# Performance work log

Measured on AMD Instinct MI355X. Metric: run time of the kernel, lower is better.

The kernel has to match this reference:

```python
import jax, jax.numpy as jnp
import numpy as np

N_NODES = 50000
N_EDGES = 500000
D_IN = 128
D_HID = 128
OUTPUT_DIM = 10.0


def gcn_conv(x, src, dst, edge_weight, W, b, n_nodes):
    # PyG GCNConv: out = D^{-1/2} (A + I) D^{-1/2} X W + b, self-loop weight 1
    xw = x @ W  # [N, D_out]
    # degree at target nodes, including self-loop weight 1
    deg = jax.ops.segment_sum(edge_weight, dst, num_segments=n_nodes) + 1.0
    dinv = jnp.where(deg > 0, jax.lax.rsqrt(deg), 0.0)  # [N]
    norm = dinv[src] * edge_weight * dinv[dst]  # [E]
    msgs = xw[src] * norm[:, None]  # [E, D_out] gathered+scaled messages
    agg = jax.ops.segment_sum(msgs, dst, num_segments=n_nodes)
    # analytic self-loop contribution: norm_ii = dinv_i * 1 * dinv_i
    agg = agg + xw * (dinv * dinv)[:, None]
    return agg + b


def setup_inputs() -> dict:
    key = jax.random.key(0)
    k = jax.random.split(key, 8)
    x = jax.random.normal(k[0], (N_NODES, D_IN), dtype=jnp.float32)
    edge_index = jax.random.randint(k[1], (2, N_EDGES), 0, N_NODES, dtype=jnp.int64)
    edge_weight = jax.random.uniform(k[2], (N_EDGES,), dtype=jnp.float32)
    s1 = 1.0 / np.sqrt(D_IN)
    s2 = 1.0 / np.sqrt(D_HID)
    W1 = jax.random.uniform(k[3], (D_IN, D_HID), minval=-s1, maxval=s1, dtype=jnp.float32)
    b1 = jnp.zeros((D_HID,), dtype=jnp.float32)
    W2 = jax.random.uniform(k[4], (D_HID, D_HID), minval=-s2, maxval=s2, dtype=jnp.float32)
    b2 = jnp.zeros((D_HID,), dtype=jnp.float32)
    Wf = jax.random.uniform(k[5], (D_HID, 1), minval=-s2, maxval=s2, dtype=jnp.float32)
    bf = jax.random.uniform(k[6], (1,), minval=-s2, maxval=s2, dtype=jnp.float32)
    return {"x": x, "edge_index": edge_index, "edge_weight": edge_weight,
            "W1": W1, "b1": b1, "W2": W2, "b2": b2, "Wf": Wf, "bf": bf}


def reference(x, edge_index, edge_weight, W1, b1, W2, b2, Wf, bf):
    src, dst = edge_index[0], edge_index[1]
    h = gcn_conv(x, src, dst, edge_weight, W1, b1, N_NODES)
    h = gcn_conv(h, src, dst, edge_weight, W2, b2, N_NODES)
    out = h @ Wf + bf  # [N, 1]
    return jax.nn.sigmoid(out) * OUTPUT_DIM
```

## Files before the change

### kernel.cpp

```cpp
#include <hip/hip_runtime.h>

#define N_NODES 50000
#define N_EDGES 500000
#define D 128
#define FXS 4194304.0f
#define CAP 64

typedef unsigned long long u64;

__global__ void pass1_kernel(const int* __restrict__ src, const int* __restrict__ dst,
                             const float* __restrict__ ew,
                             const float* __restrict__ W1, const float* __restrict__ W2,
                             const float* __restrict__ b1, const float* __restrict__ b2,
                             const float* __restrict__ Wf, const float* __restrict__ bf,
                             u64* __restrict__ degcnt, int2* __restrict__ pairs,
                             float* __restrict__ v, float* __restrict__ consts,
                             int eb) {
    if ((int)blockIdx.x == eb) {
        __shared__ float u[D];
        int t = threadIdx.x;
        if (t < D) {
            float a = 0.f;
#pragma unroll 8
            for (int j = 0; j < D; ++j) a += W2[t * D + j] * Wf[j];
            u[t] = a;
        }
        __syncthreads();
        if (t < D) {
            float a = 0.f;
#pragma unroll 8
            for (int k = 0; k < D; ++k) a += W1[t * D + k] * u[k];
            v[t] = a;
        }
        if (t == 0) {
            float c = 0.f;
            for (int k = 0; k < D; ++k) c += b1[k] * u[k];
            consts[0] = c;
        } else if (t == 1) {
            float c = bf[0];
            for (int k = 0; k < D; ++k) c += b2[k] * Wf[k];
            consts[1] = c;
        }
        return;
    }
    int e = blockIdx.x * blockDim.x + threadIdx.x;
    if (e < N_EDGES) {
        int d = dst[e];
        float w = ew[e];
        unsigned fx = __float2uint_rn(w * FXS);
        u64 old = atomicAdd(&degcnt[d], (1ull << 32) | (u64)fx);
        int slot = (int)(old >> 32);
        if (slot < CAP)
            pairs[d * CAP + slot] = make_int2(src[e], __float_as_int(w));
    }
}

__global__ void gemv_kernel(const float* __restrict__ x, const float* __restrict__ v,
                            const u64* __restrict__ degcnt,
                            float* __restrict__ dinv, float* __restrict__ tw,
                            int* __restrict__ cntv) {
    __shared__ float vs[D];
    const int t = threadIdx.x;
    if (t < D) vs[t] = v[t];
    __syncthreads();
    const int lane = t & 63;
    const int n = blockIdx.x * 4 + (t >> 6);
    float2 xv = ((const float2*)(x + (size_t)n * D))[lane];
    float a = xv.x * vs[lane * 2] + xv.y * vs[lane * 2 + 1];
#pragma unroll
    for (int off = 32; off > 0; off >>= 1) a += __shfl_xor(a, off);
    if (lane == 0) {
        u64 dc = degcnt[n];
        int c = (int)(dc >> 32);
        float deg = (float)(unsigned)(dc & 0xffffffffu) * (1.0f / FXS);
        float di = rsqrtf(deg + 1.0f);
        dinv[n] = di;
        cntv[n] = (c < CAP) ? c : CAP;
        tw[n] = di * a;
    }
}

__global__ void gather_s_kernel(const float* __restrict__ tw, const float* __restrict__ dinv,
                                const int* __restrict__ cntv, const int2* __restrict__ pairs,
                                const float* __restrict__ consts, float* __restrict__ sw) {
    int tid = threadIdx.x;
    int n = blockIdx.x * 32 + (tid >> 3);
    int l = tid & 7;
    if (n >= N_NODES) return;
    int cnt = cntv[n];
    const int2* row = pairs + (size_t)n * CAP;
    float acc = 0.f;
    for (int i = l; i < cnt; i += 8) {
        int2 p = row[i];
        acc += __int_as_float(p.y) * tw[p.x];
    }
    acc += __shfl_xor(acc, 1);
    acc += __shfl_xor(acc, 2);
    acc += __shfl_xor(acc, 4);
    if (l == 0) {
        float di = dinv[n];
        float s = di * (acc + tw[n]) + consts[0];
        sw[n] = di * s;
    }
}

__global__ void gather_z_kernel(const float* __restrict__ sw, const float* __restrict__ dinv,
                                const int* __restrict__ cntv, const int2* __restrict__ pairs,
                                const float* __restrict__ consts, float* __restrict__ out) {
    int tid = threadIdx.x;
    int n = blockIdx.x * 32 + (tid >> 3);
    int l = tid & 7;
    if (n >= N_NODES) return;
    int cnt = cntv[n];
    const int2* row = pairs + (size_t)n * CAP;
    float acc = 0.f;
    for (int i = l; i < cnt; i += 8) {
        int2 p = row[i];
        acc += __int_as_float(p.y) * sw[p.x];
    }
    acc += __shfl_xor(acc, 1);
    acc += __shfl_xor(acc, 2);
    acc += __shfl_xor(acc, 4);
    if (l == 0) {
        float di = dinv[n];
        float z = di * (acc + sw[n]) + consts[1];
        out[n] = 10.0f / (1.0f + expf(-z));
    }
}

extern "C" void kernel_launch(void* const* d_in, const int* in_sizes, int n_in,
                              void* d_out, int out_size, void* d_ws, size_t ws_size,
                              hipStream_t stream) {
    const float* x  = (const float*)d_in[0];
    const int*   ei = (const int*)d_in[1];
    const float* ew = (const float*)d_in[2];
    const float* W1 = (const float*)d_in[3];
    const float* b1 = (const float*)d_in[4];
    const float* W2 = (const float*)d_in[5];
    const float* b2 = (const float*)d_in[6];
    const float* Wf = (const float*)d_in[7];
    const float* bf = (const float*)d_in[8];
    const int* srcv = ei;
    const int* dstv = ei + N_EDGES;
    float* out = (float*)d_out;

    char* p = (char*)d_ws;
    auto alloc = [&](size_t bytes) { void* r = (void*)p; p += (bytes + 255) & ~(size_t)255; return r; };
    u64*   degcnt = (u64*)alloc((size_t)N_NODES * 8);
    float* dinv   = (float*)alloc(N_NODES * 4);
    int*   cntv   = (int*)alloc(N_NODES * 4);
    float* tw     = (float*)alloc(N_NODES * 4);
    float* sw     = (float*)alloc(N_NODES * 4);
    float* v      = (float*)alloc(D * 4);
    float* consts = (float*)alloc(2 * 4);
    int2*  pairs  = (int2*)alloc((size_t)N_NODES * CAP * 8);

    const int EB = (N_EDGES + 255) / 256;

    hipMemsetAsync(degcnt, 0, (size_t)N_NODES * 8, stream);

    pass1_kernel<<<EB + 1, 256, 0, stream>>>(srcv, dstv, ew, W1, W2, b1, b2, Wf, bf,
                                             degcnt, pairs, v, consts, EB);

    gemv_kernel<<<N_NODES / 4, 256, 0, stream>>>(x, v, degcnt, dinv, tw, cntv);

    gather_s_kernel<<<(N_NODES + 31) / 32, 256, 0, stream>>>(tw, dinv, cntv, pairs, consts, sw);
    gather_z_kernel<<<(N_NODES + 31) / 32, 256, 0, stream>>>(sw, dinv, cntv, pairs, consts, out);
}
```

Measured before the change: 136.7 us.

## Replace bucketed CSR gather with per-edge atomic scatter for both propagation passes

Drops the per-destination fixed-capacity pair buckets and the 64-bit combined degree/count atomics. Each propagation now runs as an edge-parallel float atomicAdd scatter into a zeroed accumulator, followed by a small per-node finish kernel. This removes the 25.6 MB bucket write and the strided bucket reads. In exchange it adds two more launches and float atomics, which make the summation order nondeterministic, and it re-reads src, dst and ew on every pass.

```diff
diff --git a/kernel.cpp b/kernel.cpp
--- a/kernel.cpp
+++ b/kernel.cpp
@@ -4,18 +4,13 @@
 #define N_EDGES 500000
 #define D 128
 #define FXS 4194304.0f
-#define CAP 64
 
-typedef unsigned long long u64;
-
-__global__ void pass1_kernel(const int* __restrict__ src, const int* __restrict__ dst,
-                             const float* __restrict__ ew,
+__global__ void pass1_kernel(const int* __restrict__ dst, const float* __restrict__ ew,
                              const float* __restrict__ W1, const float* __restrict__ W2,
                              const float* __restrict__ b1, const float* __restrict__ b2,
                              const float* __restrict__ Wf, const float* __restrict__ bf,
-                             u64* __restrict__ degcnt, int2* __restrict__ pairs,
-                             float* __restrict__ v, float* __restrict__ consts,
-                             int eb) {
+                             unsigned* __restrict__ deg, float* __restrict__ v,
+                             float* __restrict__ consts, int eb) {
     if ((int)blockIdx.x == eb) {
         __shared__ float u[D];
         int t = threadIdx.x;
@@ -45,20 +40,14 @@
     }
     int e = blockIdx.x * blockDim.x + threadIdx.x;
     if (e < N_EDGES) {
-        int d = dst[e];
-        float w = ew[e];
-        unsigned fx = __float2uint_rn(w * FXS);
-        u64 old = atomicAdd(&degcnt[d], (1ull << 32) | (u64)fx);
-        int slot = (int)(old >> 32);
-        if (slot < CAP)
-            pairs[d * CAP + slot] = make_int2(src[e], __float_as_int(w));
+        unsigned fx = __float2uint_rn(ew[e] * FXS);
+        atomicAdd(&deg[dst[e]], fx);
     }
 }
 
 __global__ void gemv_kernel(const float* __restrict__ x, const float* __restrict__ v,
-                            const u64* __restrict__ degcnt,
-                            float* __restrict__ dinv, float* __restrict__ tw,
-                            int* __restrict__ cntv) {
+                            const unsigned* __restrict__ deg,
+                            float* __restrict__ dinv, float* __restrict__ tw) {
     __shared__ float vs[D];
     const int t = threadIdx.x;
     if (t < D) vs[t] = v[t];
@@ -70,60 +59,38 @@
 #pragma unroll
     for (int off = 32; off > 0; off >>= 1) a += __shfl_xor(a, off);
     if (lane == 0) {
-        u64 dc = degcnt[n];
-        int c = (int)(dc >> 32);
-        float deg = (float)(unsigned)(dc & 0xffffffffu) * (1.0f / FXS);
-        float di = rsqrtf(deg + 1.0f);
+        float dg = (float)deg[n] * (1.0f / FXS);
+        float di = rsqrtf(dg + 1.0f);
         dinv[n] = di;
-        cntv[n] = (c < CAP) ? c : CAP;
         tw[n] = di * a;
     }
 }
 
-__global__ void gather_s_kernel(const float* __restrict__ tw, const float* __restrict__ dinv,
-                                const int* __restrict__ cntv, const int2* __restrict__ pairs,
-                                const float* __restrict__ consts, float* __restrict__ sw) {
-    int tid = threadIdx.x;
-    int n = blockIdx.x * 32 + (tid >> 3);
-    int l = tid & 7;
-    if (n >= N_NODES) return;
-    int cnt = cntv[n];
-    const int2* row = pairs + (size_t)n * CAP;
-    float acc = 0.f;
-    for (int i = l; i < cnt; i += 8) {
-        int2 p = row[i];
-        acc += __int_as_float(p.y) * tw[p.x];
-    }
-    acc += __shfl_xor(acc, 1);
-    acc += __shfl_xor(acc, 2);
-    acc += __shfl_xor(acc, 4);
-    if (l == 0) {
+__global__ void scatter_kernel(const int* __restrict__ src, const int* __restrict__ dst,
+                               const float* __restrict__ ew, const float* __restrict__ val,
+                               float* __restrict__ acc) {
+    int e = blockIdx.x * blockDim.x + threadIdx.x;
+    if (e < N_EDGES)
+        atomicAdd(&acc[dst[e]], ew[e] * val[src[e]]);
+}
+
+__global__ void finish_s_kernel(const float* __restrict__ acc, const float* __restrict__ tw,
+                                const float* __restrict__ dinv, const float* __restrict__ consts,
+                                float* __restrict__ sw) {
+    int n = blockIdx.x * blockDim.x + threadIdx.x;
+    if (n < N_NODES) {
         float di = dinv[n];
-        float s = di * (acc + tw[n]) + consts[0];
-        sw[n] = di * s;
+        sw[n] = di * (di * (acc[n] + tw[n]) + consts[0]);
     }
 }
 
-__global__ void gather_z_kernel(const float* __restrict__ sw, const float* __restrict__ dinv,
-                                const int* __restrict__ cntv, const int2* __restrict__ pairs,
-                                const float* __restrict__ consts, float* __restrict__ out) {
-    int tid = threadIdx.x;
-    int n = blockIdx.x * 32 + (tid >> 3);
-    int l = tid & 7;
-    if (n >= N_NODES) return;
-    int cnt = cntv[n];
-    const int2* row = pairs + (size_t)n * CAP;
-    float acc = 0.f;
-    for (int i = l; i < cnt; i += 8) {
-        int2 p = row[i];
-        acc += __int_as_float(p.y) * sw[p.x];
-    }
-    acc += __shfl_xor(acc, 1);
-    acc += __shfl_xor(acc, 2);
-    acc += __shfl_xor(acc, 4);
-    if (l == 0) {
+__global__ void finish_z_kernel(const float* __restrict__ acc, const float* __restrict__ sw,
+                                const float* __restrict__ dinv, const float* __restrict__ consts,
+                                float* __restrict__ out) {
+    int n = blockIdx.x * blockDim.x + threadIdx.x;
+    if (n < N_NODES) {
         float di = dinv[n];
-        float z = di * (acc + sw[n]) + consts[1];
+        float z = di * (acc[n] + sw[n]) + consts[1];
         out[n] = 10.0f / (1.0f + expf(-z));
     }
 }
@@ -146,24 +113,30 @@
 
     char* p = (char*)d_ws;
     auto alloc = [&](size_t bytes) { void* r = (void*)p; p += (bytes + 255) & ~(size_t)255; return r; };
-    u64*   degcnt = (u64*)alloc((size_t)N_NODES * 8);
+    char* zbase = p;
+    unsigned* deg   = (unsigned*)alloc(N_NODES * 4);
+    float*    acc_s = (float*)alloc(N_NODES * 4);
+    float*    acc_z = (float*)alloc(N_NODES * 4);
+    size_t zbytes = (size_t)(p - zbase);
     float* dinv   = (float*)alloc(N_NODES * 4);
-    int*   cntv   = (int*)alloc(N_NODES * 4);
     float* tw     = (float*)alloc(N_NODES * 4);
     float* sw     = (float*)alloc(N_NODES * 4);
     float* v      = (float*)alloc(D * 4);
     float* consts = (float*)alloc(2 * 4);
-    int2*  pairs  = (int2*)alloc((size_t)N_NODES * CAP * 8);
 
     const int EB = (N_EDGES + 255) / 256;
+    const int NB = (N_NODES + 255) / 256;
 
-    hipMemsetAsync(degcnt, 0, (size_t)N_NODES * 8, stream);
+    hipMemsetAsync(zbase, 0, zbytes, stream);
 
-    pass1_kernel<<<EB + 1, 256, 0, stream>>>(srcv, dstv, ew, W1, W2, b1, b2, Wf, bf,
-                                             degcnt, pairs, v, consts, EB);
+    pass1_kernel<<<EB + 1, 256, 0, stream>>>(dstv, ew, W1, W2, b1, b2, Wf, bf,
+                                             deg, v, consts, EB);
 
-    gemv_kernel<<<N_NODES / 4, 256, 0, stream>>>(x, v, degcnt, dinv, tw, cntv);
+    gemv_kernel<<<N_NODES / 4, 256, 0, stream>>>(x, v, deg, dinv, tw);
 
-    gather_s_kernel<<<(N_NODES + 31) / 32, 256, 0, stream>>>(tw, dinv, cntv, pairs, consts, sw);
-    gather_z_kernel<<<(N_NODES + 31) / 32, 256, 0, stream>>>(sw, dinv, cntv, pairs, consts, out);
+    scatter_kernel<<<EB, 256, 0, stream>>>(srcv, dstv, ew, tw, acc_s);
+    finish_s_kernel<<<NB, 256, 0, stream>>>(acc_s, tw, dinv, consts, sw);
+
+    scatter_kernel<<<EB, 256, 0, stream>>>(srcv, dstv, ew, sw, acc_z);
+    finish_z_kernel<<<NB, 256, 0, stream>>>(acc_z, sw, dinv, consts, out);
 }
```

After: 183.5 us. 1.34x slower.
